# Kernel optimization log

Measured on AMD Instinct MI355X. Metric: run time of the kernel, lower is better.

## Reference

```python
import jax, jax.numpy as jnp
import numpy as np

B = 16          # graphs per batch
T = 50          # cell types
C = 200         # neurons per cell type
N = T * C       # nodes per graph (10000)
NT = B * N      # total nodes (160000)
FEAT = 1        # num_node_features (forced to 1 by module structure)
H = 8           # attention heads
DEG = 32
E = NT * DEG    # edges (5.12M)
PASSES = 4
PERSIST = 1.0
EPS = 1e-5
TAU = 1.0
SLOPE = 0.2


def setup_inputs() -> dict:
    key = jax.random.key(0)
    ks = jax.random.split(key, 12)
    x = jax.random.normal(ks[0], (NT, FEAT), dtype=jnp.float32)
    # sprinkle exact zeros so the noise-injection branch is exercised
    x = jnp.where(jax.random.uniform(ks[1], x.shape) < 0.1, 0.0, x)
    # edges stay within each graph (batched disjoint graphs)
    dst = jax.random.randint(ks[2], (E,), 0, NT)
    src = (dst // N) * N + jax.random.randint(ks[3], (E,), 0, N)
    edge_index = jnp.stack([src, dst]).astype(jnp.int32)
    batch = (jnp.arange(NT) // N).astype(jnp.int32)
    perm_weights = jax.random.normal(ks[4], (T, B, C, C), dtype=jnp.float32)
    decision_vec = (jax.random.uniform(ks[5], (N,)) < 0.2).astype(jnp.float32)
    gat_w = jax.random.normal(ks[6], (FEAT, H), dtype=jnp.float32)
    att_src = jax.random.normal(ks[7], (H,), dtype=jnp.float32)
    att_dst = jax.random.normal(ks[8], (H,), dtype=jnp.float32)
    return {
        "x": x, "edge_index": edge_index, "batch": batch,
        "perm_weights": perm_weights, "decision_vec": decision_vec,
        "gat_w": gat_w, "att_src": att_src, "att_dst": att_dst,
        "gat_bias": jnp.zeros((1,), jnp.float32),
        "bn_gamma": jnp.ones((1,), jnp.float32),
        "bn_beta": jnp.zeros((1,), jnp.float32),
        "bn_mean": jnp.zeros((1,), jnp.float32),
        "bn_var": jnp.ones((1,), jnp.float32),
        "lin_w": jax.random.normal(ks[9], (1, 1), dtype=jnp.float32),
        "lin_b": jax.random.normal(ks[10], (1,), dtype=jnp.float32),
    }


def _permutation_layer(x, perm_weights, key):
    # x: [NT, FEAT] -> per-type blocks [T, B, C, FEAT]
    xb = x.reshape(B, T, C, FEAT).transpose(1, 0, 2, 3)
    u = jax.random.uniform(key, perm_weights.shape, minval=1e-10, maxval=1.0)
    gumbel = -jnp.log(-jnp.log(u))
    # F.gumbel_softmax(weights, dim=1) on [B,C,C] -> softmax over row axis (axis=2 here)
    soft = jax.nn.softmax((perm_weights + gumbel) / TAU, axis=2)
    y = jnp.einsum('tbij,tbjf->tbif', soft, xb)
    return y.transpose(1, 0, 2, 3).reshape(NT, FEAT)


def _add_noise(x, key):
    nz = x != 0
    n = nz.sum().astype(x.dtype)
    mean = jnp.sum(jnp.where(nz, x, 0.0)) / n
    var = jnp.sum(jnp.where(nz, (x - mean) ** 2, 0.0)) / (n - 1.0)  # unbiased, as torch .std()
    std = jnp.sqrt(var)
    noise = (std / 100.0) * jax.random.normal(key, x.shape, dtype=x.dtype)
    return jnp.where(nz, x, noise)


def _gat_conv(x, src, dst, gat_w, att_src, att_dst, gat_bias):
    xs = x @ gat_w                                   # [NT, H] (out_channels=1 per head)
    a_src = xs * att_src                             # [NT, H]
    a_dst = xs * att_dst
    e = a_src[src] + a_dst[dst]                      # [E+NT, H]
    e = jnp.where(e > 0, e, SLOPE * e)               # leaky_relu(0.2)
    emax = jax.ops.segment_max(e, dst, num_segments=NT)
    ee = jnp.exp(e - emax[dst])
    denom = jax.ops.segment_sum(ee, dst, num_segments=NT)
    alpha = ee / denom[dst]
    out = jax.ops.segment_sum(alpha * xs[src], dst, num_segments=NT)  # [NT, H]
    return out.mean(axis=1, keepdims=True) + gat_bias  # concat=False -> mean over heads


def reference(x, edge_index, batch, perm_weights, decision_vec, gat_w, att_src,
              att_dst, gat_bias, bn_gamma, bn_beta, bn_mean, bn_var, lin_w, lin_b):
    rk = jax.random.key(42)
    x = _permutation_layer(x, perm_weights, jax.random.fold_in(rk, 0))
    x_res = x
    x = _add_noise(x, jax.random.fold_in(rk, 1))
    # GATConv adds self loops by default
    loops = jnp.arange(NT, dtype=edge_index.dtype)
    src = jnp.concatenate([edge_index[0], loops])
    dst = jnp.concatenate([edge_index[1], loops])
    for i in range(PASSES):
        x = _gat_conv(x, src, dst, gat_w, att_src, att_dst, gat_bias)
        x = (x - bn_mean) / jnp.sqrt(bn_var + EPS) * bn_gamma + bn_beta  # eval BN
        x = jax.nn.silu(x)
        # dropout is identity in eval mode
        x = x + x_res * (PERSIST ** i)
    mask = jnp.tile(decision_vec, B)[:, None]        # [NT, 1]
    x = x * mask
    pooled = jax.ops.segment_max(x, batch, num_segments=B)  # global_max_pool -> [B, 1]
    return jax.nn.relu(pooled @ lin_w.T + lin_b)
```

## Files before the change

### kernel.cpp

```cpp
#include <hip/hip_runtime.h>
#include <stdint.h>
#include <math.h>

#define B_   16
#define T_   50
#define C_   200
#define N_   10000
#define NT_  160000
#define H_   8
#define E_   5120000
#define EPS_ 1e-5f
#define NB_  625
#define EB_  256
#define EPB_ 20000
#define GB_  40
#define GC_  250
#define JC_  5
#define JW_  40
#define ROWP_ 41
#define LOG2E_ 1.44269504088896340736f

__device__ __forceinline__ float ex2(float x){
  float r; asm("v_exp_f32 %0, %1" : "=v"(r) : "v"(x)); return r;
}

struct TF2C { unsigned a, b; };
constexpr unsigned rotl32c(unsigned v, int r){ return (v << r) | (v >> (32 - r)); }
constexpr TF2C tf_const(unsigned k0, unsigned k1, unsigned x0, unsigned x1){
  unsigned ks2 = k0 ^ k1 ^ 0x1BD11BDAu;
  unsigned ks[3] = {k0, k1, ks2};
  x0 += k0; x1 += k1;
  const int RA[4] = {13, 15, 26, 6};
  const int RB[4] = {17, 29, 16, 24};
  for (int g = 0; g < 5; ++g){
    for (int r = 0; r < 4; ++r){
      int rr = (g & 1) ? RB[r] : RA[r];
      x0 += x1; x1 = rotl32c(x1, rr); x1 ^= x0;
    }
    x0 += ks[(g + 1) % 3];
    x1 += ks[(g + 2) % 3] + (unsigned)(g + 1);
  }
  return TF2C{x0, x1};
}
constexpr TF2C KG = tf_const(0u, 42u, 0u, 0u);
constexpr TF2C KN = tf_const(0u, 42u, 0u, 1u);

__device__ __forceinline__ void tf2(unsigned k0, unsigned k1, unsigned x0, unsigned x1,
                                    unsigned &o0, unsigned &o1){
  unsigned ks2 = k0 ^ k1 ^ 0x1BD11BDAu;
  x0 += k0; x1 += k1;
#define TFR_(R) { x0 += x1; x1 = __builtin_rotateleft32(x1, R); x1 ^= x0; }
  TFR_(13) TFR_(15) TFR_(26) TFR_(6)  x0 += k1;  x1 += ks2 + 1u;
  TFR_(17) TFR_(29) TFR_(16) TFR_(24) x0 += ks2; x1 += k0 + 2u;
  TFR_(13) TFR_(15) TFR_(26) TFR_(6)  x0 += k0;  x1 += k1 + 3u;
  TFR_(17) TFR_(29) TFR_(16) TFR_(24) x0 += k1;  x1 += ks2 + 4u;
  TFR_(13) TFR_(15) TFR_(26) TFR_(6)  x0 += ks2; x1 += k0 + 5u;
#undef TFR_
  o0 = x0; o1 = x1;
}
__device__ __forceinline__ unsigned rbits(unsigned ka, unsigned kb, unsigned m){
  unsigned a, b; tf2(ka, kb, 0u, m, a, b); return a ^ b;
}

__device__ __forceinline__ float erfinv_xla(float x){
  float w = -log1pf(-x * x);
  float p;
  if (w < 5.0f){
    w = w - 2.5f;
    p = 2.81022636e-08f;
    p = fmaf(p, w, 3.43273939e-07f);
    p = fmaf(p, w, -3.5233877e-06f);
    p = fmaf(p, w, -4.39150654e-06f);
    p = fmaf(p, w, 0.00021858087f);
    p = fmaf(p, w, -0.00125372503f);
    p = fmaf(p, w, -0.00417768164f);
    p = fmaf(p, w, 0.246640727f);
    p = fmaf(p, w, 1.50140941f);
  } else {
    w = sqrtf(w) - 3.0f;
    p = -0.000200214257f;
    p = fmaf(p, w, 0.000100950558f);
    p = fmaf(p, w, 0.00134934322f);
    p = fmaf(p, w, -0.00367342844f);
    p = fmaf(p, w, 0.00573950773f);
    p = fmaf(p, w, -0.0076224613f);
    p = fmaf(p, w, 0.00943887047f);
    p = fmaf(p, w, 1.00167406f);
    p = fmaf(p, w, 2.83297682f);
  }
  return p * x;
}

__global__ __launch_bounds__(256)
void k_hist(const int* __restrict__ dst, int* __restrict__ cnt){
  __shared__ int h[NB_];
  int tid = threadIdx.x, blk = blockIdx.x;
  for (int i = tid; i < NB_; i += 256) h[i] = 0;
  __syncthreads();
  int e0 = blk * EPB_;
  for (int i = tid; i < EPB_; i += 256)
    atomicAdd(&h[dst[e0 + i] >> 8], 1);
  __syncthreads();
  for (int i = tid; i < NB_; i += 256) cnt[blk * NB_ + i] = h[i];
}

__global__ __launch_bounds__(256)
void k_sumb(const int* __restrict__ cnt, int* __restrict__ bsum){
  __shared__ int sred[4];
  int b = blockIdx.x, tid = threadIdx.x;
  int v = cnt[tid * NB_ + b];
#pragma unroll
  for (int s = 32; s >= 1; s >>= 1) v += __shfl_xor(v, s, 64);
  int w = tid >> 6, l = tid & 63;
  if (l == 0) sred[w] = v;
  __syncthreads();
  if (tid == 0) bsum[b] = sred[0] + sred[1] + sred[2] + sred[3];
}

__global__ void k_scanb(const int* __restrict__ bsum, int* __restrict__ boff){
  __shared__ int ts[256];
  int tid = threadIdx.x;
  int i0 = tid * 3;
  int c0 = (i0 + 0 < NB_) ? bsum[i0 + 0] : 0;
  int c1 = (i0 + 1 < NB_) ? bsum[i0 + 1] : 0;
  int c2 = (i0 + 2 < NB_) ? bsum[i0 + 2] : 0;
  int s = c0 + c1 + c2;
  ts[tid] = s;
  __syncthreads();
  for (int d = 1; d < 256; d <<= 1){
    int t = (tid >= d) ? ts[tid - d] : 0;
    __syncthreads();
    ts[tid] += t;
    __syncthreads();
  }
  int run = ts[tid] - s;
  if (i0 + 0 <= NB_){ boff[i0 + 0] = run; run += c0; }
  if (i0 + 1 <= NB_){ boff[i0 + 1] = run; run += c1; }
  if (i0 + 2 <= NB_){ boff[i0 + 2] = run; run += c2; }
}

__global__ __launch_bounds__(256)
void k_scanc(const int* __restrict__ cnt, const int* __restrict__ boff,
             int* __restrict__ gscan){
  __shared__ int ts[256];
  int b = blockIdx.x, tid = threadIdx.x;
  int v = cnt[tid * NB_ + b];
  ts[tid] = v;
  __syncthreads();
  for (int d = 1; d < 256; d <<= 1){
    int t = (tid >= d) ? ts[tid - d] : 0;
    __syncthreads();
    ts[tid] += t;
    __syncthreads();
  }
  gscan[tid * NB_ + b] = boff[b] + ts[tid] - v;
}

__global__ __launch_bounds__(256)
void k_append(const int* __restrict__ src, const int* __restrict__ dst,
              const int* __restrict__ gscan, unsigned* __restrict__ ebuf){
  __shared__ int gb[NB_];
  __shared__ int lc[NB_];
  int tid = threadIdx.x, blk = blockIdx.x;
  for (int i = tid; i < NB_; i += 256){ gb[i] = gscan[blk * NB_ + i]; lc[i] = 0; }
  __syncthreads();
  int e0 = blk * EPB_;
  for (int i = tid; i < EPB_; i += 256){
    int e = e0 + i;
    int d = dst[e];
    int b = d >> 8;
    int r = atomicAdd(&lc[b], 1);
    ebuf[gb[b] + r] = ((unsigned)src[e] << 8) | (unsigned)(d & 255);
  }
}

__global__ __launch_bounds__(256)
void k_bcsr(const int* __restrict__ boff, const unsigned* __restrict__ ebuf,
            int* __restrict__ offs, unsigned short* __restrict__ srcs16){
  __shared__ int cnt[256];
  __shared__ int ts[256];
  int b = blockIdx.x, tid = threadIdx.x;
  int e0 = boff[b], e1 = boff[b + 1];
  int base_node = b * 256;
  int offA = (base_node / N_) * N_;
  int boundary = offA + N_;
  cnt[tid] = 0;
  __syncthreads();
  for (int e = e0 + tid; e < e1; e += 256)
    atomicAdd(&cnt[ebuf[e] & 255u], 1);
  __syncthreads();
  int v = cnt[tid];
  ts[tid] = v;
  __syncthreads();
  for (int d = 1; d < 256; d <<= 1){
    int t = (tid >= d) ? ts[tid - d] : 0;
    __syncthreads();
    ts[tid] += t;
    __syncthreads();
  }
  int excl = ts[tid] - v;
  offs[base_node + tid] = e0 + excl;
  __syncthreads();
  cnt[tid] = excl;
  __syncthreads();
  for (int e = e0 + tid; e < e1; e += 256){
    unsigned pk = ebuf[e];
    int dl = (int)(pk & 255u);
    int goff = (base_node + dl >= boundary) ? boundary : offA;
    int pos = e0 + atomicAdd(&cnt[dl], 1);
    srcs16[pos] = (unsigned short)((int)(pk >> 8) - goff);
  }
  if (b == 0 && tid == 0) offs[NT_] = E_;
}

__global__ __launch_bounds__(512, 8)
void k_perm(const float* __restrict__ W, const float* __restrict__ x,
            float* __restrict__ ypart){
  __shared__ float ez[C_ * ROWP_];
  __shared__ float Ssh[JW_];
  __shared__ float rs[JW_];

  const int bid = blockIdx.x;
  const int tb = bid / JC_;
  const int jc = bid - tb * JC_;
  const int t = tb / B_;
  const int b = tb - t * B_;
  const int j0 = jc * JW_;
  const int xoff = (b * T_ + t) * C_;
  const int tid = threadIdx.x;
  const int w = tid >> 6, l = tid & 63;

  {
    int i = tid / JW_;
    int jj = tid - i * JW_;
    unsigned m = (unsigned)(tb * (C_ * C_) + i * C_ + j0 + jj);
    int la = i * ROWP_ + jj;
    int niter = (C_ * JW_ - tid + 511) >> 9;
    for (int it = 0; it < niter; ++it){
      unsigned bits = rbits(KG.a, KG.b, m);
      float f = __uint_as_float((bits >> 9) | 0x3f800000u) - 1.0f;
      float tneg;
      if (f >= 0.875f){
        float d = 1.0f - f;
        float p = 0.16666667f;
        p = fmaf(p, d, 0.2f);
        p = fmaf(p, d, 0.25f);
        p = fmaf(p, d, 0.33333333f);
        p = fmaf(p, d, 0.5f);
        p = fmaf(p, d, 1.0f);
        tneg = d * p;
      } else {
        float u = f + 1e-10f;
        tneg = -__logf(u);
      }
      ez[la] = __expf(W[m]) * __builtin_amdgcn_rcpf(tneg);
      jj += 32;
      int wrap = jj >= JW_;
      jj = wrap ? jj - JW_ : jj;
      m += wrap ? 2592u : 2432u;
      la += wrap ? 525 : 524;
    }
  }
  __syncthreads();

#pragma unroll
  for (int q = 0; q < 5; ++q){
    int jj = w * 5 + q;
    float s = ez[l * ROWP_ + jj] + ez[(l + 64) * ROWP_ + jj] + ez[(l + 128) * ROWP_ + jj]
            + ((l < 8) ? ez[(l + 192) * ROWP_ + jj] : 0.f);
#pragma unroll
    for (int sh = 32; sh >= 1; sh >>= 1) s += __shfl_xor(s, sh, 64);
    if (l == 0) Ssh[jj] = s;
  }
  __syncthreads();
  if (tid < JW_) rs[tid] = x[xoff + j0 + tid] / Ssh[tid];
  __syncthreads();

  if (tid < C_){
    float acc = 0.f;
#pragma unroll 8
    for (int jj = 0; jj < JW_; ++jj)
      acc = fmaf(ez[tid * ROWP_ + jj], rs[jj], acc);
    ypart[jc * NT_ + xoff + tid] = acc;
  }
}

__global__ __launch_bounds__(256)
void k_ycomb(const float* __restrict__ ypart, float* __restrict__ y,
             float* __restrict__ spart){
  __shared__ float sred[12];
  int n = blockIdx.x * 256 + threadIdx.x;
  float v = 0.f;
#pragma unroll
  for (int jc = 0; jc < JC_; ++jc) v += ypart[jc * NT_ + n];
  y[n] = v;
  float s = 0.f, c = 0.f, q = 0.f;
  if (v != 0.f){ s = v; c = 1.f; q = v * v; }
#pragma unroll
  for (int sh = 32; sh >= 1; sh >>= 1){
    s += __shfl_xor(s, sh, 64);
    c += __shfl_xor(c, sh, 64);
    q += __shfl_xor(q, sh, 64);
  }
  int w = threadIdx.x >> 6, l = threadIdx.x & 63;
  if (l == 0){ sred[w] = s; sred[4 + w] = c; sred[8 + w] = q; }
  __syncthreads();
  if (threadIdx.x == 0){
    spart[blockIdx.x * 3 + 0] = sred[0] + sred[1] + sred[2] + sred[3];
    spart[blockIdx.x * 3 + 1] = sred[4] + sred[5] + sred[6] + sred[7];
    spart[blockIdx.x * 3 + 2] = sred[8] + sred[9] + sred[10] + sred[11];
  }
}

__global__ void k_stat2(const float* __restrict__ spart, float* __restrict__ stats){
  __shared__ float sred[12];
  int tid = threadIdx.x;
  float s = 0.f, c = 0.f, q = 0.f;
  for (int i = tid; i < 625; i += 256){
    s += spart[i * 3 + 0];
    c += spart[i * 3 + 1];
    q += spart[i * 3 + 2];
  }
#pragma unroll
  for (int sh = 32; sh >= 1; sh >>= 1){
    s += __shfl_xor(s, sh, 64);
    c += __shfl_xor(c, sh, 64);
    q += __shfl_xor(q, sh, 64);
  }
  int w = tid >> 6, l = tid & 63;
  if (l == 0){ sred[w] = s; sred[4 + w] = c; sred[8 + w] = q; }
  __syncthreads();
  if (tid == 0){
    float S = sred[0] + sred[1] + sred[2] + sred[3];
    float C = sred[4] + sred[5] + sred[6] + sred[7];
    float Q = sred[8] + sred[9] + sred[10] + sred[11];
    float var = (Q - S * S / C) / (C - 1.f);
    stats[0] = sqrtf(var) * 0.01f;
  }
}

__global__ void k_noise(const float* __restrict__ y, const float* __restrict__ stats,
                        float* __restrict__ x0){
  int n = blockIdx.x * 256 + threadIdx.x;
  float v = y[n];
  if (v != 0.0f){ x0[n] = v; return; }
  float scale = stats[0];
  unsigned bits = rbits(KN.a, KN.b, (unsigned)n);
  float f = __uint_as_float((bits >> 9) | 0x3f800000u) - 1.0f;
  float u = f * 2.0f + (-0.99999994f);
  u = fmaxf(-0.99999994f, u);
  float nrm = 1.41421356237f * erfinv_xla(u);
  x0[n] = scale * nrm;
}

__global__ __launch_bounds__(256)
void k_gat(const float* __restrict__ xin, const float* __restrict__ xres,
           const int* __restrict__ offs, const unsigned short* __restrict__ srcs16,
           const float* __restrict__ gw, const float* __restrict__ asrc,
           const float* __restrict__ adst, const float* __restrict__ gbias,
           const float* __restrict__ bng, const float* __restrict__ bnb,
           const float* __restrict__ bnm, const float* __restrict__ bnv,
           float* __restrict__ xout){
  __shared__ float xsh[N_];
  int g = blockIdx.x / GB_, c = blockIdx.x - g * GB_;
  int tid = threadIdx.x;
  const float4* xv = (const float4*)(xin + g * N_);
  for (int i = tid; i < N_ / 4; i += 256) ((float4*)xsh)[i] = xv[i];
  __syncthreads();
  if (tid >= GC_) return;

  int nl = c * GC_ + tid;
  int n = g * N_ + nl;
  float xn = xsh[nl];

  float cs[H_], cdxn[H_], wv[H_];
#pragma unroll
  for (int h = 0; h < H_; ++h){
    wv[h] = gw[h];
    cs[h] = wv[h] * asrc[h] * LOG2E_;
    cdxn[h] = wv[h] * adst[h] * xn * LOG2E_;
  }
  float mh[H_], den[H_], num[H_];
#pragma unroll
  for (int h = 0; h < H_; ++h){
    float v = cs[h] * xn + cdxn[h];
    v = fmaxf(v, 0.2f * v);
    mh[h] = v; den[h] = 1.f; num[h] = xn;
  }
  int e0 = offs[n], e1 = offs[n + 1];
  for (int e = e0; e < e1; ++e){
    float xs = xsh[srcs16[e]];
#pragma unroll
    for (int h = 0; h < H_; ++h){
      float v = fmaf(cs[h], xs, cdxn[h]);
      v = fmaxf(v, 0.2f * v);
      float d = v - mh[h];
      float ed = ex2(-fabsf(d));
      bool newmax = d > 0.f;
      float corr = newmax ? ed : 1.f;
      float p    = newmax ? 1.f : ed;
      mh[h] = newmax ? v : mh[h];
      den[h] = fmaf(den[h], corr, p);
      num[h] = fmaf(num[h], corr, p * xs);
    }
  }
  float o = 0.f;
#pragma unroll
  for (int h = 0; h < H_; ++h) o += wv[h] * num[h] * __builtin_amdgcn_rcpf(den[h]);
  o = o * 0.125f + gbias[0];
  o = (o - bnm[0]) / sqrtf(bnv[0] + EPS_) * bng[0] + bnb[0];
  o = o / (1.0f + __expf(-o));
  xout[n] = o + xres[n];
}

__global__ __launch_bounds__(256)
void k_pool1(const float* __restrict__ xf, const float* __restrict__ dv,
             float* __restrict__ pmax){
  __shared__ float sred[4];
  int g = blockIdx.x / GB_, c = blockIdx.x - g * GB_;
  int tid = threadIdx.x;
  float m = -INFINITY;
  if (tid < GC_){
    int nl = c * GC_ + tid;
    m = xf[g * N_ + nl] * dv[nl];
  }
#pragma unroll
  for (int s = 32; s >= 1; s >>= 1) m = fmaxf(m, __shfl_xor(m, s, 64));
  int w = tid >> 6, l = tid & 63;
  if (l == 0) sred[w] = m;
  __syncthreads();
  if (tid == 0)
    pmax[blockIdx.x] = fmaxf(fmaxf(sred[0], sred[1]), fmaxf(sred[2], sred[3]));
}

__global__ void k_pool2(const float* __restrict__ pmax, const float* __restrict__ lw,
                        const float* __restrict__ lb, float* __restrict__ out){
  int b = blockIdx.x, l = threadIdx.x;
  float m = (l < GB_) ? pmax[b * GB_ + l] : -INFINITY;
#pragma unroll
  for (int s = 32; s >= 1; s >>= 1) m = fmaxf(m, __shfl_xor(m, s, 64));
  if (l == 0){
    float o = m * lw[0] + lb[0];
    out[b] = (o > 0.f) ? o : 0.f;
  }
}

extern "C" void kernel_launch(void* const* d_in, const int* in_sizes, int n_in,
                              void* d_out, int out_size, void* d_ws, size_t ws_size,
                              hipStream_t stream){
  const float* x     = (const float*)d_in[0];
  const int*   ei    = (const int*)d_in[1];
  const float* W     = (const float*)d_in[3];
  const float* dv    = (const float*)d_in[4];
  const float* gw    = (const float*)d_in[5];
  const float* asrc  = (const float*)d_in[6];
  const float* adst  = (const float*)d_in[7];
  const float* gbias = (const float*)d_in[8];
  const float* bng   = (const float*)d_in[9];
  const float* bnb   = (const float*)d_in[10];
  const float* bnm   = (const float*)d_in[11];
  const float* bnv   = (const float*)d_in[12];
  const float* lw    = (const float*)d_in[13];
  const float* lb    = (const float*)d_in[14];
  float* out = (float*)d_out;

  char* ws = (char*)d_ws;
  int*            offs   = (int*)           (ws + 0);
  unsigned short* srcs16 = (unsigned short*)(ws + 640256);
  int*            cnt    = (int*)           (ws + 10880256);
  int*            gscan  = (int*)           (ws + 11520256);
  unsigned*       ebuf   = (unsigned*)      (ws + 21120256);
  float*          ypart  = (float*)         (ws + 21120256);
  float*          y      = (float*)         (ws + 41600256);
  float*          x0     = (float*)         (ws + 42240256);
  float*          x1     = (float*)         (ws + 42880256);
  int*            bsum   = (int*)           (ws + 43520256);
  int*            boff   = (int*)           (ws + 43522816);
  float*          pmax   = (float*)         (ws + 43525376);
  float*          stats  = (float*)         (ws + 43527936);
  float*          spart  = (float*)         (ws + 43527968);
  if (ws_size < (size_t)43535500) return;

  const int* esrc = ei;
  const int* edst = ei + E_;

  k_hist  <<<EB_, 256, 0, stream>>>(edst, cnt);
  k_sumb  <<<NB_, 256, 0, stream>>>(cnt, bsum);
  k_scanb <<<1, 256, 0, stream>>>(bsum, boff);
  k_scanc <<<NB_, 256, 0, stream>>>(cnt, boff, gscan);
  k_append<<<EB_, 256, 0, stream>>>(esrc, edst, gscan, ebuf);
  k_bcsr  <<<NB_, 256, 0, stream>>>(boff, ebuf, offs, srcs16);
  k_perm  <<<T_ * B_ * JC_, 512, 0, stream>>>(W, x, ypart);
  k_ycomb <<<625, 256, 0, stream>>>(ypart, y, spart);
  k_stat2 <<<1, 256, 0, stream>>>(spart, stats);
  k_noise <<<625, 256, 0, stream>>>(y, stats, x0);
  k_gat<<<B_ * GB_, 256, 0, stream>>>(x0, y, offs, srcs16, gw, asrc, adst, gbias, bng, bnb, bnm, bnv, x1);
  k_gat<<<B_ * GB_, 256, 0, stream>>>(x1, y, offs, srcs16, gw, asrc, adst, gbias, bng, bnb, bnm, bnv, x0);
  k_gat<<<B_ * GB_, 256, 0, stream>>>(x0, y, offs, srcs16, gw, asrc, adst, gbias, bng, bnb, bnm, bnv, x1);
  k_gat<<<B_ * GB_, 256, 0, stream>>>(x1, y, offs, srcs16, gw, asrc, adst, gbias, bng, bnb, bnm, bnv, x0);
  k_pool1 <<<B_ * GB_, 256, 0, stream>>>(x0, dv, pmax);
  k_pool2 <<<B_, 64, 0, stream>>>(pmax, lw, lb, out);
}
```

Measured before the change: 360.6 us.

## Stage edge bucketing in shared memory and double block count in CSR build

The edge-append kernel now does a local histogram and scan of its chunk, scatters packed edges into shared memory by bucket, then writes each bucket to global memory as a contiguous wave-wide copy. This replaces random per-edge global scatter writes with coalesced ones. Edge chunks are halved (512 blocks of 1024 threads), and the count, scan and sum kernels are resized to 512 threads to match. The append kernel reads dst twice and uses about 45KB of LDS, which may limit occupancy.

```diff
diff --git a/kernel.cpp b/kernel.cpp
--- a/kernel.cpp
+++ b/kernel.cpp
@@ -11,8 +11,9 @@
 #define E_   5120000
 #define EPS_ 1e-5f
 #define NB_  625
-#define EB_  256
-#define EPB_ 20000
+#define EB_  512
+#define EPB_ 10000
+#define ATH_ 1024
 #define GB_  40
 #define GC_  250
 #define JC_  5
@@ -91,22 +92,22 @@
   return p * x;
 }
 
-__global__ __launch_bounds__(256)
+__global__ __launch_bounds__(ATH_)
 void k_hist(const int* __restrict__ dst, int* __restrict__ cnt){
   __shared__ int h[NB_];
   int tid = threadIdx.x, blk = blockIdx.x;
-  for (int i = tid; i < NB_; i += 256) h[i] = 0;
+  for (int i = tid; i < NB_; i += ATH_) h[i] = 0;
   __syncthreads();
   int e0 = blk * EPB_;
-  for (int i = tid; i < EPB_; i += 256)
+  for (int i = tid; i < EPB_; i += ATH_)
     atomicAdd(&h[dst[e0 + i] >> 8], 1);
   __syncthreads();
-  for (int i = tid; i < NB_; i += 256) cnt[blk * NB_ + i] = h[i];
-}
-
-__global__ __launch_bounds__(256)
+  for (int i = tid; i < NB_; i += ATH_) cnt[blk * NB_ + i] = h[i];
+}
+
+__global__ __launch_bounds__(512)
 void k_sumb(const int* __restrict__ cnt, int* __restrict__ bsum){
-  __shared__ int sred[4];
+  __shared__ int sred[8];
   int b = blockIdx.x, tid = threadIdx.x;
   int v = cnt[tid * NB_ + b];
 #pragma unroll
@@ -114,7 +115,12 @@
   int w = tid >> 6, l = tid & 63;
   if (l == 0) sred[w] = v;
   __syncthreads();
-  if (tid == 0) bsum[b] = sred[0] + sred[1] + sred[2] + sred[3];
+  if (tid == 0){
+    int t = 0;
+#pragma unroll
+    for (int i = 0; i < 8; ++i) t += sred[i];
+    bsum[b] = t;
+  }
 }
 
 __global__ void k_scanb(const int* __restrict__ bsum, int* __restrict__ boff){
@@ -139,15 +145,15 @@
   if (i0 + 2 <= NB_){ boff[i0 + 2] = run; run += c2; }
 }
 
-__global__ __launch_bounds__(256)
+__global__ __launch_bounds__(512)
 void k_scanc(const int* __restrict__ cnt, const int* __restrict__ boff,
              int* __restrict__ gscan){
-  __shared__ int ts[256];
+  __shared__ int ts[512];
   int b = blockIdx.x, tid = threadIdx.x;
   int v = cnt[tid * NB_ + b];
   ts[tid] = v;
   __syncthreads();
-  for (int d = 1; d < 256; d <<= 1){
+  for (int d = 1; d < 512; d <<= 1){
     int t = (tid >= d) ? ts[tid - d] : 0;
     __syncthreads();
     ts[tid] += t;
@@ -156,21 +162,45 @@
   gscan[tid * NB_ + b] = boff[b] + ts[tid] - v;
 }
 
-__global__ __launch_bounds__(256)
+__global__ __launch_bounds__(ATH_)
 void k_append(const int* __restrict__ src, const int* __restrict__ dst,
               const int* __restrict__ gscan, unsigned* __restrict__ ebuf){
-  __shared__ int gb[NB_];
-  __shared__ int lc[NB_];
+  __shared__ unsigned esh[EPB_];
+  __shared__ int hist[NB_];
+  __shared__ int loff[NB_ + 1];
   int tid = threadIdx.x, blk = blockIdx.x;
-  for (int i = tid; i < NB_; i += 256){ gb[i] = gscan[blk * NB_ + i]; lc[i] = 0; }
-  __syncthreads();
   int e0 = blk * EPB_;
-  for (int i = tid; i < EPB_; i += 256){
+  for (int i = tid; i < NB_; i += ATH_) hist[i] = 0;
+  __syncthreads();
+  for (int i = tid; i < EPB_; i += ATH_)
+    atomicAdd(&hist[dst[e0 + i] >> 8], 1);
+  __syncthreads();
+  if (tid < NB_) loff[tid + 1] = hist[tid];
+  if (tid == 0) loff[0] = 0;
+  __syncthreads();
+  for (int d = 1; d < NB_; d <<= 1){
+    int v = 0;
+    if (tid < NB_ && tid >= d) v = loff[tid + 1 - d];
+    __syncthreads();
+    if (tid < NB_ && tid >= d) loff[tid + 1] += v;
+    __syncthreads();
+  }
+  for (int i = tid; i < NB_; i += ATH_) hist[i] = 0;
+  __syncthreads();
+  for (int i = tid; i < EPB_; i += ATH_){
     int e = e0 + i;
     int d = dst[e];
     int b = d >> 8;
-    int r = atomicAdd(&lc[b], 1);
-    ebuf[gb[b] + r] = ((unsigned)src[e] << 8) | (unsigned)(d & 255);
+    int p = loff[b] + atomicAdd(&hist[b], 1);
+    esh[p] = ((unsigned)src[e] << 8) | (unsigned)(d & 255);
+  }
+  __syncthreads();
+  int wv = tid >> 6, ln = tid & 63;
+  for (int b = wv; b < NB_; b += ATH_ / 64){
+    int lo = loff[b], len = loff[b + 1] - lo;
+    int gb0 = gscan[blk * NB_ + b];
+    for (int p = ln; p < len; p += 64)
+      ebuf[gb0 + p] = esh[lo + p];
   }
 }
 
@@ -468,7 +498,7 @@
   int*            offs   = (int*)           (ws + 0);
   unsigned short* srcs16 = (unsigned short*)(ws + 640256);
   int*            cnt    = (int*)           (ws + 10880256);
-  int*            gscan  = (int*)           (ws + 11520256);
+  int*            gscan  = (int*)           (ws + 12160256);
   unsigned*       ebuf   = (unsigned*)      (ws + 21120256);
   float*          ypart  = (float*)         (ws + 21120256);
   float*          y      = (float*)         (ws + 41600256);
@@ -484,11 +514,11 @@
   const int* esrc = ei;
   const int* edst = ei + E_;
 
-  k_hist  <<<EB_, 256, 0, stream>>>(edst, cnt);
-  k_sumb  <<<NB_, 256, 0, stream>>>(cnt, bsum);
+  k_hist  <<<EB_, ATH_, 0, stream>>>(edst, cnt);
+  k_sumb  <<<NB_, 512, 0, stream>>>(cnt, bsum);
   k_scanb <<<1, 256, 0, stream>>>(bsum, boff);
-  k_scanc <<<NB_, 256, 0, stream>>>(cnt, boff, gscan);
-  k_append<<<EB_, 256, 0, stream>>>(esrc, edst, gscan, ebuf);
+  k_scanc <<<NB_, 512, 0, stream>>>(cnt, boff, gscan);
+  k_append<<<EB_, ATH_, 0, stream>>>(esrc, edst, gscan, ebuf);
   k_bcsr  <<<NB_, 256, 0, stream>>>(boff, ebuf, offs, srcs16);
   k_perm  <<<T_ * B_ * JC_, 512, 0, stream>>>(W, x, ypart);
   k_ycomb <<<625, 256, 0, stream>>>(ypart, y, spart);
```

Result: faster. 325.9 us (-9.6%).
